# Optimization experiments

Hardware: AMD Instinct MI355X
Metric: run time of the kernel (lower is better)

Reference implementation:

```python
import jax, jax.numpy as jnp
import numpy as np

V = 200000   # total vertices
K = 96       # neighbours per vertex (incl. self)
NSEG = 4     # number of row-split segments


def setup_inputs() -> dict:
    key = jax.random.key(0)
    k1, k2 = jax.random.split(key)
    seg_size = V // NSEG
    row_splits = (jnp.arange(NSEG + 1, dtype=jnp.int32) * seg_size)
    seg_id = jnp.repeat(jnp.arange(NSEG, dtype=jnp.int32), seg_size)
    seg_start = row_splits[seg_id]                      # (V,)
    # segment-local random neighbours, self index in column 0 (kNN convention)
    offs = jax.random.randint(k1, (V, K), 0, seg_size, dtype=jnp.int32)
    neighs = seg_start[:, None] + offs
    neighs = neighs.at[:, 0].set(jnp.arange(V, dtype=jnp.int32))
    hier = jax.random.uniform(k2, (V, 1), dtype=jnp.float32)
    return {"neighs": neighs, "hier": hier, "row_splits": row_splits}


def _cluster(neighs, hier, row_splits):
    """Greedy hierarchy-ordered neighbour clustering (NMS-like).

    Returns:
      sel     (V,1) int32: cluster-centre vertex indices, compacted to the
              front in processing order, padded with -1 (original op returns
              a dynamically sized tensor; we pad for fixed shapes).
      rs      (n_seg+1,) int32: row splits after selection.
      ggather (V,1) int32: for each vertex, the position in `sel` of its
              cluster centre (gather-back indices).
    """
    Vn, _ = neighs.shape
    n_seg = row_splits.shape[0] - 1
    seg_id = jnp.searchsorted(row_splits[1:], jnp.arange(Vn), side='right').astype(jnp.int32)
    # per-segment argsort descending on hier, with global offsets == global
    # lexsort by (segment, -hier) since vertices are segment-contiguous
    order = jnp.lexsort((-hier[:, 0], seg_id)).astype(jnp.int32)  # (V,)

    def step(assign, v):
        is_new = assign[v] < 0                 # v not yet absorbed -> new centre
        nb = neighs[v]                          # (K,) neighbour indices
        grab = is_new & (assign[nb] < 0)        # unassigned neighbours get taken
        assign = assign.at[jnp.where(is_new, v, Vn)].set(v, mode='drop')
        assign = assign.at[jnp.where(grab, nb, Vn)].set(v, mode='drop')
        return assign, is_new

    assign0 = jnp.full((Vn,), -1, jnp.int32)
    assign, is_new = jax.lax.scan(step, assign0, order)  # assign: centre vertex per vertex

    new_i = is_new.astype(jnp.int32)
    pos = jnp.cumsum(new_i) - 1                           # rank of each centre in order
    sel = jnp.full((Vn,), -1, jnp.int32).at[jnp.where(is_new, pos, Vn)].set(order, mode='drop')
    counts = jax.ops.segment_sum(new_i, seg_id[order], num_segments=n_seg)
    rs = jnp.concatenate([jnp.zeros((1,), jnp.int32), jnp.cumsum(counts).astype(jnp.int32)])
    center_rank = jnp.zeros((Vn,), jnp.int32).at[jnp.where(is_new, order, Vn)].set(pos, mode='drop')
    ggather = center_rank[assign].reshape(-1, 1)
    return sel.reshape(-1, 1), rs, ggather


def reference(neighs, hier, row_splits):
    return _cluster(neighs, hier, row_splits)
```

## Files before the change

kernel.cpp:

```cpp
#include <hip/hip_runtime.h>

#define IDX_BITS 20
#define IDX_MASK ((1u << IDX_BITS) - 1)
#define NT1 1024
#define MAX_G1 512
#define T1 49152
#define TB2 16
#define T2 1536
#define GRID_ROUND_CAP 16
#define MAX_ROUNDS 8000
#define SC_CAP 1024
#define SV_CAP 4096

typedef unsigned long long u64;

__device__ __forceinline__ u64 pack_key(float h, int v) {
  return ((u64)(~__float_as_uint(h)) << IDX_BITS) | (unsigned)v;
}

__device__ __forceinline__ int ald(const int* p) {
  return __hip_atomic_load((int*)p, __ATOMIC_RELAXED, __HIP_MEMORY_SCOPE_AGENT);
}
__device__ __forceinline__ u64 ald64(const u64* p) {
  return __hip_atomic_load((u64*)p, __ATOMIC_RELAXED, __HIP_MEMORY_SCOPE_AGENT);
}
__device__ __forceinline__ void ast(int* p, int v) {
  __hip_atomic_store(p, v, __ATOMIC_RELAXED, __HIP_MEMORY_SCOPE_AGENT);
}

struct Ctx {
  const int* __restrict__ neighs;
  const float* __restrict__ hier;
  const int* __restrict__ row_splits;
  int V, K, nseg;
  u64* assign;
  int* tag;
  int* listA;
  int* listB;
  u64* centre_key;
  int* centre_v;
  int* rank_of;
  int* cnt;
  int* out_sel;
  int* out_rs;
  int* out_gg;
};

struct BlkState {
  int sc_cnt, sv_cnt, sc_base, sv_base;
  int seg_hist[8];
  int sc_list[SC_CAP];
  int sv_list[SV_CAP];
};

__device__ __forceinline__ void xbar(int* bar, int target) {
  __syncthreads();
  if (threadIdx.x == 0) {
    __hip_atomic_fetch_add(bar, 1, __ATOMIC_RELAXED, __HIP_MEMORY_SCOPE_AGENT);
    while (__hip_atomic_load(bar, __ATOMIC_RELAXED, __HIP_MEMORY_SCOPE_AGENT) < target)
      __builtin_amdgcn_s_sleep(2);
  }
  __syncthreads();
}

__device__ __forceinline__ void record_direct(const Ctx& c, int v, u64 pv) {
  int slot = atomicAdd(&c.cnt[4], 1);
  int seg = 0;
  for (int t = 1; t < c.nseg; ++t) seg += (v >= c.row_splits[t]);
  c.centre_v[slot] = v;
  c.centre_key[slot] = ((u64)seg << 52) | pv;
  atomicAdd(&c.cnt[8 + seg], 1);
}

__device__ __forceinline__ void phaseB(const Ctx& c, const int* rl, int an, int r,
                                       int qs, int qst, int ql) {
  if (c.K == 96) {
    for (int i = qs; i < an; i += qst) {
      int u = rl ? ald(&rl[i]) : i;
      u64 pu = pack_key(c.hier[u], u);
      if (rl && ald64(&c.assign[u]) <= pu) continue;
      const int* row = c.neighs + (size_t)u * 96;
      int w[6];
#pragma unroll
      for (int t = 0; t < 6; ++t) w[t] = row[ql + 16 * t];
#pragma unroll
      for (int t = 0; t < 6; ++t)
        if (pack_key(c.hier[w[t]], w[t]) > pu) ast(&c.tag[w[t]], r);
    }
  } else {
    for (int i = qs; i < an; i += qst) {
      int u = rl ? ald(&rl[i]) : i;
      u64 pu = pack_key(c.hier[u], u);
      if (rl && ald64(&c.assign[u]) <= pu) continue;
      const int* row = c.neighs + (size_t)u * c.K;
      for (int j = ql; j < c.K; j += 16) {
        int w = row[j];
        if (pack_key(c.hier[w], w) > pu) ast(&c.tag[w], r);
      }
    }
  }
}

__device__ __forceinline__ void phaseC(const Ctx& c, BlkState& bs, const int* rl,
                                       int* wl, int* survc, int an, int r,
                                       int qs, int qst, int ql) {
  for (int i = qs; i < an; i += qst) {
    int u = rl ? ald(&rl[i]) : i;
    u64 pu = pack_key(c.hier[u], u);
    if (ald64(&c.assign[u]) <= pu) continue;
    if (ald(&c.tag[u]) != r) {
      const int* row = c.neighs + (size_t)u * c.K;
      if (c.K == 96) {
#pragma unroll
        for (int t = 0; t < 6; ++t) atomicMin(&c.assign[row[ql + 16 * t]], pu);
      } else {
        for (int j = ql; j < c.K; j += 16) atomicMin(&c.assign[row[j]], pu);
      }
      if (ql == 0) {
        int s = atomicAdd(&bs.sc_cnt, 1);
        if (s < SC_CAP) bs.sc_list[s] = u; else record_direct(c, u, pu);
      }
    } else if (ql == 0) {
      u64 y = ald64(&c.assign[u]);
      if (y > pu) {
        int s = atomicAdd(&bs.sv_cnt, 1);
        if (s < SV_CAP) bs.sv_list[s] = u;
        else { int g = atomicAdd(survc, 1); ast(&wl[g], u); }
      }
    }
  }
}

__device__ __forceinline__ void flush_block(const Ctx& c, BlkState& bs, int* wl, int* survc) {
  __syncthreads();
  int nsc = min(bs.sc_cnt, SC_CAP), nsv = min(bs.sv_cnt, SV_CAP);
  if (threadIdx.x == 0 && nsc) bs.sc_base = atomicAdd(&c.cnt[4], nsc);
  if (threadIdx.x == 0 && nsv) bs.sv_base = atomicAdd(survc, nsv);
  if (threadIdx.x < 8) bs.seg_hist[threadIdx.x] = 0;
  __syncthreads();
  for (int i = threadIdx.x; i < nsv; i += blockDim.x) ast(&wl[bs.sv_base + i], bs.sv_list[i]);
  for (int i = threadIdx.x; i < nsc; i += blockDim.x) {
    int v = bs.sc_list[i];
    int seg = 0;
    for (int t = 1; t < c.nseg; ++t) seg += (v >= c.row_splits[t]);
    c.centre_v[bs.sc_base + i] = v;
    c.centre_key[bs.sc_base + i] = ((u64)seg << 52) | pack_key(c.hier[v], v);
    atomicAdd(&bs.seg_hist[seg], 1);
  }
  __syncthreads();
  if (threadIdx.x < c.nseg) {
    int h = bs.seg_hist[threadIdx.x];
    if (h) atomicAdd(&c.cnt[8 + threadIdx.x], h);
  }
  __syncthreads();
  if (threadIdx.x == 0) { bs.sc_cnt = 0; bs.sv_cnt = 0; }
}

__global__ void __launch_bounds__(NT1) k_tier1(Ctx c) {
  __shared__ BlkState bs;
  const int tid = blockIdx.x * blockDim.x + threadIdx.x;
  const int nthr = gridDim.x * blockDim.x;
  const int ql = threadIdx.x & 15;
  const int qg = tid >> 4, nq = nthr >> 4;
  const int nb = gridDim.x;
  if (threadIdx.x == 0) { bs.sc_cnt = 0; bs.sv_cnt = 0; }
  __syncthreads();

  int aliveN = c.V, r = 0, ep = 0;
  while (true) {
    const int* rl = (r & 1) ? c.listA : c.listB;
    int* wl = (r & 1) ? c.listB : c.listA;
    if (tid == 0) ast(&c.cnt[(r + 1) & 1], 0);
    phaseB(c, r ? rl : nullptr, aliveN, r, qg, nq, ql);
    xbar(&c.cnt[16], nb * (++ep));
    phaseC(c, bs, r ? rl : nullptr, wl, &c.cnt[(r + 1) & 1], aliveN, r, qg, nq, ql);
    flush_block(c, bs, wl, &c.cnt[(r + 1) & 1]);
    xbar(&c.cnt[16], nb * (++ep));
    aliveN = ald(&c.cnt[(r + 1) & 1]);
    ++r;
    if (aliveN == 0 || aliveN <= T1 || r >= GRID_ROUND_CAP) break;
  }
  if (tid == 0) { ast(&c.cnt[5], aliveN); ast(&c.cnt[6], r); }
}

__global__ void __launch_bounds__(NT1) k_tier2(Ctx c) {
  __shared__ BlkState bs;
  const int ql = threadIdx.x & 15;
  const int NBQ = NT1 >> 4;
  if (threadIdx.x == 0) { bs.sc_cnt = 0; bs.sv_cnt = 0; }
  __syncthreads();

  int an = ald(&c.cnt[5]), tr = ald(&c.cnt[6]);
  if (an <= T2) return;

  const int qstart = blockIdx.x * NBQ + (threadIdx.x >> 4);
  const int qstride = TB2 * NBQ;
  int ep = 0;
  while (true) {
    const int* rl = (tr & 1) ? c.listA : c.listB;
    int* wl = (tr & 1) ? c.listB : c.listA;
    if (blockIdx.x == 0 && threadIdx.x == 0) ast(&c.cnt[(tr + 1) & 1], 0);
    phaseB(c, rl, an, tr, qstart, qstride, ql);
    xbar(&c.cnt[32], TB2 * (++ep));
    phaseC(c, bs, rl, wl, &c.cnt[(tr + 1) & 1], an, tr, qstart, qstride, ql);
    flush_block(c, bs, wl, &c.cnt[(tr + 1) & 1]);
    xbar(&c.cnt[32], TB2 * (++ep));
    an = ald(&c.cnt[(tr + 1) & 1]);
    ++tr;
    if (an == 0 || an <= T2 || tr >= MAX_ROUNDS) break;
  }
  if (blockIdx.x == 0 && threadIdx.x == 0) { ast(&c.cnt[5], an); ast(&c.cnt[6], tr); }
}

__global__ void __launch_bounds__(NT1) k_tier3(Ctx c) {
  __shared__ BlkState bs;
  const int ql = threadIdx.x & 15;
  const int bq = threadIdx.x >> 4;
  const int NBQ = NT1 >> 4;
  if (threadIdx.x == 0) { bs.sc_cnt = 0; bs.sv_cnt = 0; }
  __syncthreads();

  int an = ald(&c.cnt[5]), tr = ald(&c.cnt[6]);
  while (an > 0 && tr < MAX_ROUNDS) {
    const int* rl = (tr & 1) ? c.listA : c.listB;
    int* wl = (tr & 1) ? c.listB : c.listA;
    if (threadIdx.x == 0) ast(&c.cnt[(tr + 1) & 1], 0);
    phaseB(c, rl, an, tr, bq, NBQ, ql);
    __syncthreads();
    phaseC(c, bs, rl, wl, &c.cnt[(tr + 1) & 1], an, tr, bq, NBQ, ql);
    flush_block(c, bs, wl, &c.cnt[(tr + 1) & 1]);
    __syncthreads();
    an = ald(&c.cnt[(tr + 1) & 1]);
    ++tr;
  }
}

__global__ void __launch_bounds__(NT1) k_rank(Ctx c) {
  __shared__ u64 shp[NT1];
  const int nC = c.cnt[4];
  for (int base = blockIdx.x * NT1; base < nC; base += gridDim.x * NT1) {
    int idx = base + threadIdx.x;
    bool have = idx < nC;
    u64 mykey = have ? c.centre_key[idx] : 0;
    int myv = have ? c.centre_v[idx] : 0;
    int myrank = 0;
    for (int cs = 0; cs < nC; cs += NT1) {
      int j = cs + threadIdx.x;
      shp[threadIdx.x] = (j < nC) ? c.centre_key[j] : ~0ull;
      __syncthreads();
      int lim = min(NT1, nC - cs);
      for (int t = 0; t < lim; ++t) myrank += (shp[t] < mykey) ? 1 : 0;
      __syncthreads();
    }
    if (have) {
      c.out_sel[myrank] = myv;
      c.rank_of[myv] = myrank;
    }
  }
  if (blockIdx.x == 0 && threadIdx.x == 0) {
    int run = 0;
    c.out_rs[0] = 0;
    for (int s = 0; s < c.nseg; ++s) { run += c.cnt[8 + s]; c.out_rs[s + 1] = run; }
  }
}

__global__ void __launch_bounds__(256) k_gg(Ctx c) {
  int v = blockIdx.x * blockDim.x + threadIdx.x;
  const int stride = gridDim.x * blockDim.x;
  for (; v < c.V; v += stride) {
    u64 y = c.assign[v];
    u64 pv = pack_key(c.hier[v], v);
    int ctr = (y < pv) ? (int)(y & IDX_MASK) : v;
    c.out_gg[v] = c.rank_of[ctr];
  }
}

extern "C" void kernel_launch(void* const* d_in, const int* in_sizes, int n_in,
                              void* d_out, int out_size, void* d_ws, size_t ws_size,
                              hipStream_t stream) {
  Ctx c;
  c.neighs = (const int*)d_in[0];
  c.hier = (const float*)d_in[1];
  c.row_splits = (const int*)d_in[2];
  c.V = in_sizes[1];
  c.K = in_sizes[0] / c.V;
  c.nseg = in_sizes[2] - 1;

  char* pm = (char*)d_ws;
  const size_t V = (size_t)c.V;
  c.assign = (u64*)pm;        pm += V * 8;
  c.tag = (int*)pm;           pm += V * 4;
  size_t ff_bytes = V * 12;
  c.listA = (int*)pm;         pm += V * 4;
  c.listB = (int*)pm;         pm += V * 4;
  c.centre_key = (u64*)pm;    pm += V * 8;
  c.centre_v = (int*)pm;      pm += V * 4;
  c.rank_of = (int*)pm;       pm += V * 4;
  c.cnt = (int*)pm;           pm += 64 * 4;

  int* out = (int*)d_out;
  c.out_sel = out;
  c.out_rs = out + c.V;
  c.out_gg = out + c.V + c.nseg + 1;

  hipMemsetAsync(d_ws, 0xFF, ff_bytes, stream);
  hipMemsetAsync((void*)c.cnt, 0, 64 * 4, stream);
  hipMemsetAsync((void*)c.out_sel, 0xFF, V * 4, stream);

  int dev = 0, nCU = 0, maxB = 0;
  hipGetDevice(&dev);
  hipDeviceGetAttribute(&nCU, hipDeviceAttributeMultiprocessorCount, dev);
  hipOccupancyMaxActiveBlocksPerMultiprocessor(&maxB, k_tier1, NT1, 0);
  if (nCU <= 0) nCU = 256;
  if (maxB <= 0) maxB = 1;
  int g1 = nCU * maxB;
  if (g1 > MAX_G1) g1 = MAX_G1;

  void* args[] = { &c };
  hipLaunchCooperativeKernel((void*)k_tier1, dim3(g1), dim3(NT1), args, 0, stream);
  k_tier2<<<TB2, NT1, 0, stream>>>(c);
  k_tier3<<<1, NT1, 0, stream>>>(c);
  k_rank<<<16, NT1, 0, stream>>>(c);
  k_gg<<<512, 256, 0, stream>>>(c);
}
```

Before: 1.625 ms.

## Run final clustering tier on an LDS-resident frontier with per-round compaction

Tier 3 now holds the remaining frontier (up to 4096 vertices) in shared memory, with tag and done flags, and uses a global rank_of map to find neighbours inside the frontier. Each round compacts the survivors in LDS, so global tag and assign rereads and list writes are avoided. The handoff threshold T2 rises from 1536 to 4096, so fewer rounds need the multi-block grid barrier. A release fence is added to the grid barrier, and the tag and list stores become plain writes instead of atomic stores. The single-block tier now handles more vertices per round serially, and it returns early without doing the work if the frontier exceeds the cap.

```diff
diff --git a/kernel.cpp b/kernel.cpp
--- a/kernel.cpp
+++ b/kernel.cpp
@@ -6,7 +6,8 @@
 #define MAX_G1 512
 #define T1 49152
 #define TB2 16
-#define T2 1536
+#define T2 4096
+#define T3CAP 4096
 #define GRID_ROUND_CAP 16
 #define MAX_ROUNDS 8000
 #define SC_CAP 1024
@@ -56,6 +57,7 @@
 __device__ __forceinline__ void xbar(int* bar, int target) {
   __syncthreads();
   if (threadIdx.x == 0) {
+    __builtin_amdgcn_fence(__ATOMIC_RELEASE, "agent");
     __hip_atomic_fetch_add(bar, 1, __ATOMIC_RELAXED, __HIP_MEMORY_SCOPE_AGENT);
     while (__hip_atomic_load(bar, __ATOMIC_RELAXED, __HIP_MEMORY_SCOPE_AGENT) < target)
       __builtin_amdgcn_s_sleep(2);
@@ -85,7 +87,7 @@
       for (int t = 0; t < 6; ++t) w[t] = row[ql + 16 * t];
 #pragma unroll
       for (int t = 0; t < 6; ++t)
-        if (pack_key(c.hier[w[t]], w[t]) > pu) ast(&c.tag[w[t]], r);
+        if (pack_key(c.hier[w[t]], w[t]) > pu) c.tag[w[t]] = r;
     }
   } else {
     for (int i = qs; i < an; i += qst) {
@@ -95,7 +97,7 @@
       const int* row = c.neighs + (size_t)u * c.K;
       for (int j = ql; j < c.K; j += 16) {
         int w = row[j];
-        if (pack_key(c.hier[w], w) > pu) ast(&c.tag[w], r);
+        if (pack_key(c.hier[w], w) > pu) c.tag[w] = r;
       }
     }
   }
@@ -125,7 +127,7 @@
       if (y > pu) {
         int s = atomicAdd(&bs.sv_cnt, 1);
         if (s < SV_CAP) bs.sv_list[s] = u;
-        else { int g = atomicAdd(survc, 1); ast(&wl[g], u); }
+        else { int g = atomicAdd(survc, 1); wl[g] = u; }
       }
     }
   }
@@ -138,7 +140,7 @@
   if (threadIdx.x == 0 && nsv) bs.sv_base = atomicAdd(survc, nsv);
   if (threadIdx.x < 8) bs.seg_hist[threadIdx.x] = 0;
   __syncthreads();
-  for (int i = threadIdx.x; i < nsv; i += blockDim.x) ast(&wl[bs.sv_base + i], bs.sv_list[i]);
+  for (int i = threadIdx.x; i < nsv; i += blockDim.x) wl[bs.sv_base + i] = bs.sv_list[i];
   for (int i = threadIdx.x; i < nsc; i += blockDim.x) {
     int v = bs.sc_list[i];
     int seg = 0;
@@ -213,25 +215,79 @@
 }
 
 __global__ void __launch_bounds__(NT1) k_tier3(Ctx c) {
-  __shared__ BlkState bs;
+  __shared__ int fr[T3CAP];
+  __shared__ int tg[T3CAP];
+  __shared__ unsigned char dd[T3CAP];
+  __shared__ int tmp[T3CAP];
+  __shared__ int nnew;
   const int ql = threadIdx.x & 15;
   const int bq = threadIdx.x >> 4;
   const int NBQ = NT1 >> 4;
-  if (threadIdx.x == 0) { bs.sc_cnt = 0; bs.sv_cnt = 0; }
-  __syncthreads();
-
-  int an = ald(&c.cnt[5]), tr = ald(&c.cnt[6]);
-  while (an > 0 && tr < MAX_ROUNDS) {
-    const int* rl = (tr & 1) ? c.listA : c.listB;
-    int* wl = (tr & 1) ? c.listB : c.listA;
-    if (threadIdx.x == 0) ast(&c.cnt[(tr + 1) & 1], 0);
-    phaseB(c, rl, an, tr, bq, NBQ, ql);
-    __syncthreads();
-    phaseC(c, bs, rl, wl, &c.cnt[(tr + 1) & 1], an, tr, bq, NBQ, ql);
-    flush_block(c, bs, wl, &c.cnt[(tr + 1) & 1]);
-    __syncthreads();
-    an = ald(&c.cnt[(tr + 1) & 1]);
-    ++tr;
+
+  int an = ald(&c.cnt[5]);
+  int tr = ald(&c.cnt[6]);
+  if (an <= 0 || an > T3CAP) return;
+  const int* rl = (tr & 1) ? c.listA : c.listB;
+
+  for (int i = threadIdx.x; i < an; i += NT1) {
+    int v = ald(&rl[i]);
+    u64 pv = pack_key(c.hier[v], v);
+    fr[i] = v;
+    tg[i] = -1;
+    dd[i] = (ald64(&c.assign[v]) <= pv) ? 1 : 0;
+    c.rank_of[v] = i;
+  }
+  __syncthreads();
+
+  int r = tr;
+  while (an > 0 && r < MAX_ROUNDS) {
+    for (int i = bq; i < an; i += NBQ) {
+      if (dd[i]) continue;
+      int u = fr[i];
+      u64 pu = pack_key(c.hier[u], u);
+      const int* row = c.neighs + (size_t)u * c.K;
+      for (int j = ql; j < c.K; j += 16) {
+        int w = row[j];
+        if (pack_key(c.hier[w], w) > pu) {
+          int s = c.rank_of[w];
+          if ((unsigned)s < (unsigned)an && fr[s] == w) tg[s] = r;
+        }
+      }
+    }
+    __syncthreads();
+    for (int i = bq; i < an; i += NBQ) {
+      if (dd[i]) continue;
+      if (tg[i] != r) {
+        int u = fr[i];
+        u64 pu = pack_key(c.hier[u], u);
+        const int* row = c.neighs + (size_t)u * c.K;
+        for (int j = ql; j < c.K; j += 16) {
+          int w = row[j];
+          atomicMin(&c.assign[w], pu);
+          if (pack_key(c.hier[w], w) > pu) {
+            int s = c.rank_of[w];
+            if ((unsigned)s < (unsigned)an && fr[s] == w) dd[s] = 1;
+          }
+        }
+        if (ql == 0) { dd[i] = 1; record_direct(c, u, pu); }
+      }
+    }
+    __syncthreads();
+    if (threadIdx.x == 0) nnew = 0;
+    __syncthreads();
+    for (int i = threadIdx.x; i < an; i += NT1) {
+      if (!dd[i]) { int j = atomicAdd(&nnew, 1); tmp[j] = fr[i]; }
+    }
+    __syncthreads();
+    an = nnew;
+    __syncthreads();
+    for (int i = threadIdx.x; i < an; i += NT1) {
+      int v = tmp[i];
+      fr[i] = v; tg[i] = -1; dd[i] = 0;
+      c.rank_of[v] = i;
+    }
+    __syncthreads();
+    ++r;
   }
 }
 
```

After: 1.792 ms. 10.2% more time.

## Replace round-based tagging with dependency-count propagation of centre decisions

Applied to the files above, without the earlier changes.

The per-round scan-and-tag scheme over all alive vertices is replaced by a dependency-driven scheme. An init kernel counts, for each vertex, the neighbours that outrank it and would absorb it. Vertices with a count of zero are seeded into a worklist. Each propagation pass then only processes vertices whose status has just become decided: a centre claims and kills its lower-ranked neighbours, and a dead vertex decrements its neighbours' counts. This removes the large cooperative grid kernel and repeated full rescans, but the remaining frontier passes run on only 16 blocks and then a single block, so the number of rounds follows the dependency depth.

```diff
diff --git a/kernel.cpp b/kernel.cpp
--- a/kernel.cpp
+++ b/kernel.cpp
@@ -2,12 +2,12 @@
 
 #define IDX_BITS 20
 #define IDX_MASK ((1u << IDX_BITS) - 1)
-#define NT1 1024
-#define MAX_G1 512
-#define T1 49152
+#define DEADF (1 << 30)
+#define CLAIM_SENT (-(1 << 30))
+#define NT 1024
+#define NB_INIT 256
 #define TB2 16
 #define T2 1536
-#define GRID_ROUND_CAP 16
 #define MAX_ROUNDS 8000
 #define SC_CAP 1024
 #define SV_CAP 4096
@@ -20,9 +20,6 @@
 
 __device__ __forceinline__ int ald(const int* p) {
   return __hip_atomic_load((int*)p, __ATOMIC_RELAXED, __HIP_MEMORY_SCOPE_AGENT);
-}
-__device__ __forceinline__ u64 ald64(const u64* p) {
-  return __hip_atomic_load((u64*)p, __ATOMIC_RELAXED, __HIP_MEMORY_SCOPE_AGENT);
 }
 __device__ __forceinline__ void ast(int* p, int v) {
   __hip_atomic_store(p, v, __ATOMIC_RELAXED, __HIP_MEMORY_SCOPE_AGENT);
@@ -34,7 +31,7 @@
   const int* __restrict__ row_splits;
   int V, K, nseg;
   u64* assign;
-  int* tag;
+  int* nsmall;
   int* listA;
   int* listB;
   u64* centre_key;
@@ -72,60 +69,73 @@
   atomicAdd(&c.cnt[8 + seg], 1);
 }
 
-__device__ __forceinline__ void phaseB(const Ctx& c, const int* rl, int an, int r,
-                                       int qs, int qst, int ql) {
-  if (c.K == 96) {
-    for (int i = qs; i < an; i += qst) {
-      int u = rl ? ald(&rl[i]) : i;
-      u64 pu = pack_key(c.hier[u], u);
-      if (rl && ald64(&c.assign[u]) <= pu) continue;
-      const int* row = c.neighs + (size_t)u * 96;
-      int w[6];
+__device__ __forceinline__ void push_succ(const Ctx& c, BlkState& bs, int* wl,
+                                          int* survc, int enc) {
+  int s = atomicAdd(&bs.sv_cnt, 1);
+  if (s < SV_CAP) bs.sv_list[s] = enc;
+  else { int g = atomicAdd(survc, 1); ast(&wl[g], enc); }
+}
+
+__device__ void prop_pass(const Ctx& c, BlkState& bs, const int* rl, int* wl,
+                          int* survc, int an, int qs, int qst, int ql) {
+  for (int i = qs; i < an; i += qst) {
+    int e = ald(&rl[i]);
+    int v = e & IDX_MASK;
+    bool dead = (e & DEADF) != 0;
+    u64 pu = pack_key(c.hier[v], v);
+    if (c.K == 96) {
+      const int* row = c.neighs + (size_t)v * 96;
+      int w[6]; u64 kw[6];
 #pragma unroll
       for (int t = 0; t < 6; ++t) w[t] = row[ql + 16 * t];
 #pragma unroll
-      for (int t = 0; t < 6; ++t)
-        if (pack_key(c.hier[w[t]], w[t]) > pu) ast(&c.tag[w[t]], r);
-    }
-  } else {
-    for (int i = qs; i < an; i += qst) {
-      int u = rl ? ald(&rl[i]) : i;
-      u64 pu = pack_key(c.hier[u], u);
-      if (rl && ald64(&c.assign[u]) <= pu) continue;
-      const int* row = c.neighs + (size_t)u * c.K;
-      for (int j = ql; j < c.K; j += 16) {
-        int w = row[j];
-        if (pack_key(c.hier[w], w) > pu) ast(&c.tag[w], r);
+      for (int t = 0; t < 6; ++t) kw[t] = pack_key(c.hier[w[t]], w[t]);
+      if (!dead) {
+#pragma unroll
+        for (int t = 0; t < 6; ++t) atomicMin(&c.assign[w[t]], pu);
+#pragma unroll
+        for (int t = 0; t < 6; ++t)
+          if (kw[t] > pu) {
+            int old = atomicExch(&c.nsmall[w[t]], CLAIM_SENT);
+            if (old >= 0) push_succ(c, bs, wl, survc, w[t] | DEADF);
+          }
+        if (ql == 0) {
+          int s = atomicAdd(&bs.sc_cnt, 1);
+          if (s < SC_CAP) bs.sc_list[s] = v; else record_direct(c, v, pu);
+        }
+      } else {
+#pragma unroll
+        for (int t = 0; t < 6; ++t)
+          if (kw[t] > pu) {
+            int old = atomicAdd(&c.nsmall[w[t]], -1);
+            if (old == 1 && atomicCAS(&c.nsmall[w[t]], 0, CLAIM_SENT) == 0)
+              push_succ(c, bs, wl, survc, w[t]);
+          }
       }
-    }
-  }
-}
-
-__device__ __forceinline__ void phaseC(const Ctx& c, BlkState& bs, const int* rl,
-                                       int* wl, int* survc, int an, int r,
-                                       int qs, int qst, int ql) {
-  for (int i = qs; i < an; i += qst) {
-    int u = rl ? ald(&rl[i]) : i;
-    u64 pu = pack_key(c.hier[u], u);
-    if (ald64(&c.assign[u]) <= pu) continue;
-    if (ald(&c.tag[u]) != r) {
-      const int* row = c.neighs + (size_t)u * c.K;
-      if (c.K == 96) {
-#pragma unroll
-        for (int t = 0; t < 6; ++t) atomicMin(&c.assign[row[ql + 16 * t]], pu);
+    } else {
+      const int* row = c.neighs + (size_t)v * c.K;
+      if (!dead) {
+        for (int j = ql; j < c.K; j += 16) atomicMin(&c.assign[row[j]], pu);
+        for (int j = ql; j < c.K; j += 16) {
+          int w = row[j];
+          if (pack_key(c.hier[w], w) > pu) {
+            int old = atomicExch(&c.nsmall[w], CLAIM_SENT);
+            if (old >= 0) push_succ(c, bs, wl, survc, w | DEADF);
+          }
+        }
+        if (ql == 0) {
+          int s = atomicAdd(&bs.sc_cnt, 1);
+          if (s < SC_CAP) bs.sc_list[s] = v; else record_direct(c, v, pu);
+        }
       } else {
-        for (int j = ql; j < c.K; j += 16) atomicMin(&c.assign[row[j]], pu);
-      }
-      if (ql == 0) {
-        int s = atomicAdd(&bs.sc_cnt, 1);
-        if (s < SC_CAP) bs.sc_list[s] = u; else record_direct(c, u, pu);
-      }
-    } else if (ql == 0) {
-      u64 y = ald64(&c.assign[u]);
-      if (y > pu) {
-        int s = atomicAdd(&bs.sv_cnt, 1);
-        if (s < SV_CAP) bs.sv_list[s] = u;
-        else { int g = atomicAdd(survc, 1); ast(&wl[g], u); }
+        for (int j = ql; j < c.K; j += 16) {
+          int w = row[j];
+          if (pack_key(c.hier[w], w) > pu) {
+            int old = atomicAdd(&c.nsmall[w], -1);
+            if (old == 1 && atomicCAS(&c.nsmall[w], 0, CLAIM_SENT) == 0)
+              push_succ(c, bs, wl, survc, w);
+          }
+        }
       }
     }
   }
@@ -156,99 +166,108 @@
   if (threadIdx.x == 0) { bs.sc_cnt = 0; bs.sv_cnt = 0; }
 }
 
-__global__ void __launch_bounds__(NT1) k_tier1(Ctx c) {
+__global__ void __launch_bounds__(NT) k_init(Ctx c) {
+  const int ql = threadIdx.x & 15;
+  const int qg = (blockIdx.x * NT + threadIdx.x) >> 4;
+  const int nq = (gridDim.x * NT) >> 4;
+  if (c.K == 96) {
+    for (int v = qg; v < c.V; v += nq) {
+      u64 pv = pack_key(c.hier[v], v);
+      const int* row = c.neighs + (size_t)v * 96;
+      int w[6];
+#pragma unroll
+      for (int t = 0; t < 6; ++t) w[t] = row[ql + 16 * t];
+#pragma unroll
+      for (int t = 0; t < 6; ++t)
+        if (pack_key(c.hier[w[t]], w[t]) > pv) atomicAdd(&c.nsmall[w[t]], 1);
+    }
+  } else {
+    for (int v = qg; v < c.V; v += nq) {
+      u64 pv = pack_key(c.hier[v], v);
+      const int* row = c.neighs + (size_t)v * c.K;
+      for (int j = ql; j < c.K; j += 16) {
+        int w = row[j];
+        if (pack_key(c.hier[w], w) > pv) atomicAdd(&c.nsmall[w], 1);
+      }
+    }
+  }
+}
+
+__global__ void __launch_bounds__(NT) k_seed(Ctx c) {
   __shared__ BlkState bs;
-  const int tid = blockIdx.x * blockDim.x + threadIdx.x;
-  const int nthr = gridDim.x * blockDim.x;
-  const int ql = threadIdx.x & 15;
-  const int qg = tid >> 4, nq = nthr >> 4;
-  const int nb = gridDim.x;
   if (threadIdx.x == 0) { bs.sc_cnt = 0; bs.sv_cnt = 0; }
   __syncthreads();
-
-  int aliveN = c.V, r = 0, ep = 0;
-  while (true) {
-    const int* rl = (r & 1) ? c.listA : c.listB;
-    int* wl = (r & 1) ? c.listB : c.listA;
-    if (tid == 0) ast(&c.cnt[(r + 1) & 1], 0);
-    phaseB(c, r ? rl : nullptr, aliveN, r, qg, nq, ql);
-    xbar(&c.cnt[16], nb * (++ep));
-    phaseC(c, bs, r ? rl : nullptr, wl, &c.cnt[(r + 1) & 1], aliveN, r, qg, nq, ql);
-    flush_block(c, bs, wl, &c.cnt[(r + 1) & 1]);
-    xbar(&c.cnt[16], nb * (++ep));
-    aliveN = ald(&c.cnt[(r + 1) & 1]);
-    ++r;
-    if (aliveN == 0 || aliveN <= T1 || r >= GRID_ROUND_CAP) break;
-  }
-  if (tid == 0) { ast(&c.cnt[5], aliveN); ast(&c.cnt[6], r); }
-}
-
-__global__ void __launch_bounds__(NT1) k_tier2(Ctx c) {
+  const int gtid = blockIdx.x * NT + threadIdx.x;
+  const int nthr = gridDim.x * NT;
+  for (int v = gtid; v < c.V; v += nthr) {
+    if (ald(&c.nsmall[v]) == 0 && atomicCAS(&c.nsmall[v], 0, CLAIM_SENT) == 0)
+      push_succ(c, bs, c.listA, &c.cnt[0], v);
+  }
+  flush_block(c, bs, c.listA, &c.cnt[0]);
+}
+
+__global__ void __launch_bounds__(NT) k_t2(Ctx c) {
   __shared__ BlkState bs;
   const int ql = threadIdx.x & 15;
-  const int NBQ = NT1 >> 4;
-  if (threadIdx.x == 0) { bs.sc_cnt = 0; bs.sv_cnt = 0; }
-  __syncthreads();
-
-  int an = ald(&c.cnt[5]), tr = ald(&c.cnt[6]);
-  if (an <= T2) return;
-
+  const int NBQ = NT >> 4;
   const int qstart = blockIdx.x * NBQ + (threadIdx.x >> 4);
   const int qstride = TB2 * NBQ;
-  int ep = 0;
-  while (true) {
-    const int* rl = (tr & 1) ? c.listA : c.listB;
-    int* wl = (tr & 1) ? c.listB : c.listA;
-    if (blockIdx.x == 0 && threadIdx.x == 0) ast(&c.cnt[(tr + 1) & 1], 0);
-    phaseB(c, rl, an, tr, qstart, qstride, ql);
+  if (threadIdx.x == 0) { bs.sc_cnt = 0; bs.sv_cnt = 0; }
+  __syncthreads();
+
+  int an = ald(&c.cnt[0]), r = 0, ep = 0;
+  while (an > T2 && r < MAX_ROUNDS) {
+    const int* rl = (r & 1) ? c.listB : c.listA;
+    int* wl = (r & 1) ? c.listA : c.listB;
+    int* survc = &c.cnt[(r + 1) & 1];
+    if (blockIdx.x == 0 && threadIdx.x == 0) ast(survc, 0);
     xbar(&c.cnt[32], TB2 * (++ep));
-    phaseC(c, bs, rl, wl, &c.cnt[(tr + 1) & 1], an, tr, qstart, qstride, ql);
-    flush_block(c, bs, wl, &c.cnt[(tr + 1) & 1]);
+    prop_pass(c, bs, rl, wl, survc, an, qstart, qstride, ql);
+    flush_block(c, bs, wl, survc);
     xbar(&c.cnt[32], TB2 * (++ep));
-    an = ald(&c.cnt[(tr + 1) & 1]);
-    ++tr;
-    if (an == 0 || an <= T2 || tr >= MAX_ROUNDS) break;
-  }
-  if (blockIdx.x == 0 && threadIdx.x == 0) { ast(&c.cnt[5], an); ast(&c.cnt[6], tr); }
-}
-
-__global__ void __launch_bounds__(NT1) k_tier3(Ctx c) {
+    an = ald(survc);
+    ++r;
+  }
+  if (blockIdx.x == 0 && threadIdx.x == 0) { ast(&c.cnt[5], an); ast(&c.cnt[6], r); }
+}
+
+__global__ void __launch_bounds__(NT) k_t3(Ctx c) {
   __shared__ BlkState bs;
   const int ql = threadIdx.x & 15;
   const int bq = threadIdx.x >> 4;
-  const int NBQ = NT1 >> 4;
+  const int NBQ = NT >> 4;
   if (threadIdx.x == 0) { bs.sc_cnt = 0; bs.sv_cnt = 0; }
   __syncthreads();
 
-  int an = ald(&c.cnt[5]), tr = ald(&c.cnt[6]);
-  while (an > 0 && tr < MAX_ROUNDS) {
-    const int* rl = (tr & 1) ? c.listA : c.listB;
-    int* wl = (tr & 1) ? c.listB : c.listA;
-    if (threadIdx.x == 0) ast(&c.cnt[(tr + 1) & 1], 0);
-    phaseB(c, rl, an, tr, bq, NBQ, ql);
+  int an = ald(&c.cnt[5]), r = ald(&c.cnt[6]);
+  while (an > 0 && r < MAX_ROUNDS) {
+    const int* rl = (r & 1) ? c.listB : c.listA;
+    int* wl = (r & 1) ? c.listA : c.listB;
+    int* survc = &c.cnt[(r + 1) & 1];
+    if (threadIdx.x == 0) ast(survc, 0);
     __syncthreads();
-    phaseC(c, bs, rl, wl, &c.cnt[(tr + 1) & 1], an, tr, bq, NBQ, ql);
-    flush_block(c, bs, wl, &c.cnt[(tr + 1) & 1]);
+    prop_pass(c, bs, rl, wl, survc, an, bq, NBQ, ql);
+    flush_block(c, bs, wl, survc);
     __syncthreads();
-    an = ald(&c.cnt[(tr + 1) & 1]);
-    ++tr;
-  }
-}
-
-__global__ void __launch_bounds__(NT1) k_rank(Ctx c) {
-  __shared__ u64 shp[NT1];
+    an = ald(survc);
+    ++r;
+  }
+}
+
+__global__ void __launch_bounds__(NT) k_rank(Ctx c) {
+  __shared__ u64 shp[NT];
   const int nC = c.cnt[4];
-  for (int base = blockIdx.x * NT1; base < nC; base += gridDim.x * NT1) {
+  for (int base = blockIdx.x * NT; base < nC; base += gridDim.x * NT) {
     int idx = base + threadIdx.x;
     bool have = idx < nC;
     u64 mykey = have ? c.centre_key[idx] : 0;
     int myv = have ? c.centre_v[idx] : 0;
     int myrank = 0;
-    for (int cs = 0; cs < nC; cs += NT1) {
+    for (int cs = 0; cs < nC; cs += NT) {
       int j = cs + threadIdx.x;
       shp[threadIdx.x] = (j < nC) ? c.centre_key[j] : ~0ull;
       __syncthreads();
-      int lim = min(NT1, nC - cs);
+      int lim = min(NT, nC - cs);
       for (int t = 0; t < lim; ++t) myrank += (shp[t] < mykey) ? 1 : 0;
       __syncthreads();
     }
@@ -289,8 +308,7 @@
   char* pm = (char*)d_ws;
   const size_t V = (size_t)c.V;
   c.assign = (u64*)pm;        pm += V * 8;
-  c.tag = (int*)pm;           pm += V * 4;
-  size_t ff_bytes = V * 12;
+  c.nsmall = (int*)pm;        pm += V * 4;
   c.listA = (int*)pm;         pm += V * 4;
   c.listB = (int*)pm;         pm += V * 4;
   c.centre_key = (u64*)pm;    pm += V * 8;
@@ -303,23 +321,15 @@
   c.out_rs = out + c.V;
   c.out_gg = out + c.V + c.nseg + 1;
 
-  hipMemsetAsync(d_ws, 0xFF, ff_bytes, stream);
+  hipMemsetAsync(d_ws, 0xFF, V * 8, stream);
+  hipMemsetAsync((void*)c.nsmall, 0, V * 4, stream);
   hipMemsetAsync((void*)c.cnt, 0, 64 * 4, stream);
   hipMemsetAsync((void*)c.out_sel, 0xFF, V * 4, stream);
 
-  int dev = 0, nCU = 0, maxB = 0;
-  hipGetDevice(&dev);
-  hipDeviceGetAttribute(&nCU, hipDeviceAttributeMultiprocessorCount, dev);
-  hipOccupancyMaxActiveBlocksPerMultiprocessor(&maxB, k_tier1, NT1, 0);
-  if (nCU <= 0) nCU = 256;
-  if (maxB <= 0) maxB = 1;
-  int g1 = nCU * maxB;
-  if (g1 > MAX_G1) g1 = MAX_G1;
-
-  void* args[] = { &c };
-  hipLaunchCooperativeKernel((void*)k_tier1, dim3(g1), dim3(NT1), args, 0, stream);
-  k_tier2<<<TB2, NT1, 0, stream>>>(c);
-  k_tier3<<<1, NT1, 0, stream>>>(c);
-  k_rank<<<16, NT1, 0, stream>>>(c);
+  k_init<<<NB_INIT, NT, 0, stream>>>(c);
+  k_seed<<<NB_INIT, NT, 0, stream>>>(c);
+  k_t2<<<TB2, NT, 0, stream>>>(c);
+  k_t3<<<1, NT, 0, stream>>>(c);
+  k_rank<<<16, NT, 0, stream>>>(c);
   k_gg<<<512, 256, 0, stream>>>(c);
 }
```

After: 4.570 ms. +181.2%, slower.
